# Kernel optimization log

Hardware: AMD Instinct MI355X
Metric: run time of the kernel (lower is better)

## Reference

```python
import jax, jax.numpy as jnp
import numpy as np

NNZ = 3355443          # int(4096*4096*(1-0.8))
IN_FEATURES = 4096
OUT_FEATURES = 4096
BATCH = 64
ACTIVE_THRESHOLD = 0.01


def setup_inputs() -> dict:
    key = jax.random.key(0)
    k1, k2, k3, k4 = jax.random.split(key, 4)
    x = jax.random.uniform(k1, (BATCH, IN_FEATURES), dtype=jnp.float32)
    row_indices = jax.random.randint(k2, (NNZ,), 0, OUT_FEATURES, dtype=jnp.int32)
    col_indices = jax.random.randint(k3, (NNZ,), 0, IN_FEATURES, dtype=jnp.int32)
    values = jax.random.normal(k4, (NNZ,), dtype=jnp.float32)
    bias = jnp.zeros((OUT_FEATURES,), dtype=jnp.float32)
    return {"x": x, "row_indices": row_indices, "col_indices": col_indices,
            "values": values, "bias": bias}


def reference(x, row_indices, col_indices, values, bias):
    # Event-driven gating: only columns with x > threshold contribute.
    # Equivalent to masking x, then a standard COO spmv per batch row.
    xm = jnp.where(x > ACTIVE_THRESHOLD, x, jnp.zeros((), x.dtype))   # [B, in]
    contrib = values[None, :] * xm[:, col_indices]                    # [B, nnz]
    out = jnp.zeros((x.shape[0], bias.shape[0]), dtype=x.dtype)
    out = out.at[:, row_indices].add(contrib)                         # scatter-add over rows
    return out + bias[None, :]
```

## Files before the change

### kernel.cpp

```cpp
#include <hip/hip_runtime.h>
#include <hip/hip_bf16.h>
#include <stdint.h>

#define IN_F 4096
#define OUT_F 4096
#define NBKT 512
#define SBLOCKS 410
#define REC_PER_SB 8192
#define SMAX 7168u
#define THRESH 0.01f

typedef unsigned int u32;
typedef unsigned short u16;
typedef __attribute__((ext_vector_type(8))) short short8;
typedef __attribute__((ext_vector_type(4))) float f32x4;

static constexpr size_t pad256(size_t x) { return (x + 255u) & ~(size_t)255u; }
static constexpr size_t WS_XB   = 0;
static constexpr size_t WS_CUR  = pad256(WS_XB + (size_t)512 * 64 * 8 * 2);
static constexpr size_t WS_BINS = pad256(WS_CUR + (size_t)NBKT * 4);
static constexpr size_t WS_NEEDED = WS_BINS + (size_t)NBKT * SMAX * 4;

static __device__ __forceinline__ u16 f2bf(float v) {
  __hip_bfloat16 h = __float2bfloat16(v);
  return *reinterpret_cast<u16*>(&h);
}

__global__ __launch_bounds__(512) void k_init(u32* __restrict__ gcursor) {
  gcursor[threadIdx.x] = 0u;
}

__global__ __launch_bounds__(1024) void k_scatter(const int* __restrict__ rows,
                                                  const int* __restrict__ cols,
                                                  const float* __restrict__ vals, u32 nnz,
                                                  const float* __restrict__ x,
                                                  u16* __restrict__ xB,
                                                  u32* __restrict__ gcursor,
                                                  u32* __restrict__ sortb) {
  __shared__ u32 cnt[NBKT];
  __shared__ u32 pref[NBKT + 1];
  __shared__ u32 gbase[NBKT];
  __shared__ u32 srt[REC_PER_SB];
  __shared__ u16 srtb[REC_PER_SB];
  const int tid = threadIdx.x;
  const int lane = tid & 63;
  const int wid = tid >> 6;

  if (blockIdx.x < 32) {
    const int g = blockIdx.x * 1024 + tid;
    const int b = g & 63;
    const int kg = g >> 6;
    const float* src = x + (size_t)b * IN_F + kg * 8;
    const f32x4 a0 = *reinterpret_cast<const f32x4*>(src);
    const f32x4 a1 = *reinterpret_cast<const f32x4*>(src + 4);
    short8 o;
#pragma unroll
    for (int e = 0; e < 4; ++e) {
      float v = a0[e]; v = (v > THRESH) ? v : 0.0f; o[e] = (short)f2bf(v);
    }
#pragma unroll
    for (int e = 0; e < 4; ++e) {
      float v = a1[e]; v = (v > THRESH) ? v : 0.0f; o[4 + e] = (short)f2bf(v);
    }
    *reinterpret_cast<short8*>(xB + ((size_t)kg * 64 + b) * 8) = o;
  }

  if (tid < NBKT) cnt[tid] = 0;
  __syncthreads();
  const u32 base_i = blockIdx.x * (u32)REC_PER_SB;
  u32 rec[8], bkt[8], rk[8];
#pragma unroll
  for (int j = 0; j < 8; ++j) {
    const u32 i = base_i + (u32)j * 1024u + tid;
    bkt[j] = 0xffffffffu;
    if (i < nnz) {
      const u32 r = (u32)rows[i] & 4095u;
      const u32 c = (u32)cols[i] & 4095u;
      rec[j] = (c << 20) | ((r & 7u) << 16) | (u32)f2bf(vals[i]);
      bkt[j] = r >> 3;
      rk[j] = atomicAdd(&cnt[bkt[j]], 1u);
    }
  }
  __syncthreads();
  if (wid == 0) {
    u32 a[8]; u32 s = 0;
#pragma unroll
    for (int j = 0; j < 8; ++j) { a[j] = cnt[lane * 8 + j]; s += a[j]; }
    u32 xx = s;
#pragma unroll
    for (int d = 1; d < 64; d <<= 1) {
      const u32 y = (u32)__shfl_up((int)xx, d, 64);
      if (lane >= d) xx += y;
    }
    u32 e = xx - s;
#pragma unroll
    for (int j = 0; j < 8; ++j) { pref[lane * 8 + j] = e; e += a[j]; }
    if (lane == 63) pref[NBKT] = e;
  }
  __syncthreads();
#pragma unroll
  for (int j = 0; j < 8; ++j)
    if (bkt[j] != 0xffffffffu) {
      const u32 pos = pref[bkt[j]] + rk[j];
      srt[pos] = rec[j];
      srtb[pos] = (u16)bkt[j];
    }
  if (tid < NBKT) {
    const u32 len = pref[tid + 1] - pref[tid];
    gbase[tid] = len ? atomicAdd(&gcursor[tid], len) : 0u;
  }
  __syncthreads();
  const u32 tot = pref[NBKT];
#pragma unroll
  for (int j = 0; j < 8; ++j) {
    const u32 i = (u32)j * 1024u + tid;
    if (i < tot) {
      const u32 t = srtb[i];
      const u32 off = gbase[t] + (i - pref[t]);
      if (off < SMAX) sortb[(size_t)t * SMAX + off] = srt[i];
    }
  }
}

__global__ __launch_bounds__(1024, 4) void k_accum(const u32* __restrict__ sortb,
                                                   const u32* __restrict__ ntot,
                                                   const u16* __restrict__ xB,
                                                   const float* __restrict__ bias,
                                                   float* __restrict__ out) {
  __shared__ float W[8 * 4096];
  const int tid = threadIdx.x;
  const int lane = tid & 63;
  const int w = tid >> 6;
  const u32 t = blockIdx.x;
  u32 n = ntot[t];
  if (n > SMAX) n = SMAX;
  const u32* bin = sortb + (size_t)t * SMAX;

  const f32x4 zv = {0.f, 0.f, 0.f, 0.f};
#pragma unroll
  for (int j = 0; j < 8; ++j)
    *reinterpret_cast<f32x4*>(&W[j * 4096 + tid * 4]) = zv;
  __syncthreads();

#define ADDREC(RC) do {                                                   \
    const u32 rl_ = ((RC) >> 16) & 7u;                                    \
    const u32 cl_ = ((RC) >> 20) ^ (rl_ << 3);    \
    unsafeAtomicAdd(&W[rl_ * 4096u + cl_], __uint_as_float((RC) << 16));  \
  } while (0)
  u32 i = (u32)tid;
  for (; i + 3072u < n; i += 4096u) {
    const u32 r0 = bin[i];
    const u32 r1 = bin[i + 1024u];
    const u32 r2 = bin[i + 2048u];
    const u32 r3 = bin[i + 3072u];
    ADDREC(r0); ADDREC(r1); ADDREC(r2); ADDREC(r3);
  }
  for (; i < n; i += 1024u) { const u32 r0 = bin[i]; ADDREC(r0); }
#undef ADDREC
  __syncthreads();

  f32x4 acc0 = zv, acc1 = zv, acc2 = zv, acc3 = zv;
  const int row = lane & 15;
  const bool alive = row < 8;
  const int rw = row & 7;
  const int e8 = (lane >> 4) * 8;
#pragma unroll
  for (int s = 0; s < 8; ++s) {
    const int klb = w * 256 + s * 32 + e8;
    const int sw = klb ^ (rw << 3);
    f32x4 wa = *reinterpret_cast<const f32x4*>(&W[rw * 4096 + sw]);
    f32x4 wb = *reinterpret_cast<const f32x4*>(&W[rw * 4096 + (sw + 4)]);
    if (!alive) { wa = zv; wb = zv; }
    short8 af;
#pragma unroll
    for (int e = 0; e < 4; ++e) af[e] = (short)f2bf(wa[e]);
#pragma unroll
    for (int e = 0; e < 4; ++e) af[4 + e] = (short)f2bf(wb[e]);
    const u16* bp = xB + (size_t)(klb >> 3) * 512 + (u32)row * 8;
    const short8 b0 = *reinterpret_cast<const short8*>(bp);
    const short8 b1 = *reinterpret_cast<const short8*>(bp + 128);
    const short8 b2 = *reinterpret_cast<const short8*>(bp + 256);
    const short8 b3 = *reinterpret_cast<const short8*>(bp + 384);
    acc0 = __builtin_amdgcn_mfma_f32_16x16x32_bf16(af, b0, acc0, 0, 0, 0);
    acc1 = __builtin_amdgcn_mfma_f32_16x16x32_bf16(af, b1, acc1, 0, 0, 0);
    acc2 = __builtin_amdgcn_mfma_f32_16x16x32_bf16(af, b2, acc2, 0, 0, 0);
    acc3 = __builtin_amdgcn_mfma_f32_16x16x32_bf16(af, b3, acc3, 0, 0, 0);
  }
  __syncthreads();
  {
    const int ccol = lane & 15;
    const int rb = (lane >> 4) * 4;
    if (rb < 8) {
#pragma unroll
      for (int qq = 0; qq < 4; ++qq) W[((w * 4 + 0) * 8 + rb + qq) * 16 + ccol] = acc0[qq];
#pragma unroll
      for (int qq = 0; qq < 4; ++qq) W[((w * 4 + 1) * 8 + rb + qq) * 16 + ccol] = acc1[qq];
#pragma unroll
      for (int qq = 0; qq < 4; ++qq) W[((w * 4 + 2) * 8 + rb + qq) * 16 + ccol] = acc2[qq];
#pragma unroll
      for (int qq = 0; qq < 4; ++qq) W[((w * 4 + 3) * 8 + rb + qq) * 16 + ccol] = acc3[qq];
    }
  }
  __syncthreads();
  if (tid < 512) {
    const int rl = tid & 7;
    const int b = tid >> 3;
    float sum = bias[t * 8u + rl];
#pragma unroll
    for (int w2 = 0; w2 < 16; ++w2)
      sum += W[((w2 * 4 + (b >> 4)) * 8 + rl) * 16 + (b & 15)];
    out[(size_t)b * OUT_F + t * 8u + rl] = sum;
  }
}

__global__ __launch_bounds__(256) void k_bias_init(const float* __restrict__ bias,
                                                   float* __restrict__ out) {
  const int i = blockIdx.x * 256 + threadIdx.x;
  if (i < 64 * OUT_F) out[i] = bias[i & (OUT_F - 1)];
}

__global__ __launch_bounds__(256) void k_fallback(const int* __restrict__ rows,
                                                  const int* __restrict__ cols,
                                                  const float* __restrict__ vals,
                                                  const float* __restrict__ x,
                                                  float* __restrict__ out, int nnz) {
  const int gw = (int)(((u32)blockIdx.x * blockDim.x + threadIdx.x) >> 6);
  const int lane = threadIdx.x & 63;
  const int nw = (int)(((u32)gridDim.x * blockDim.x) >> 6);
  for (int i = gw; i < nnz; i += nw) {
    const int r = rows[i];
    const int c = cols[i];
    const float v = vals[i];
    const float xv = x[lane * IN_F + c];
    if (xv > THRESH) atomicAdd(&out[(size_t)lane * OUT_F + r], v * xv);
  }
}

extern "C" void kernel_launch(void* const* d_in, const int* in_sizes, int n_in,
                              void* d_out, int out_size, void* d_ws, size_t ws_size,
                              hipStream_t stream) {
  const float* x = (const float*)d_in[0];
  const int* rows = (const int*)d_in[1];
  const int* cols = (const int*)d_in[2];
  const float* vals = (const float*)d_in[3];
  const float* bias = (const float*)d_in[4];
  float* out = (float*)d_out;
  const int nnz = in_sizes[1];

  if (ws_size >= WS_NEEDED && nnz <= SBLOCKS * REC_PER_SB) {
    u16* xB = (u16*)((char*)d_ws + WS_XB);
    u32* gcursor = (u32*)((char*)d_ws + WS_CUR);
    u32* sortb = (u32*)((char*)d_ws + WS_BINS);
    k_init<<<1, 512, 0, stream>>>(gcursor);
    k_scatter<<<SBLOCKS, 1024, 0, stream>>>(rows, cols, vals, (u32)nnz, x, xB,
                                            gcursor, sortb);
    k_accum<<<NBKT, 1024, 0, stream>>>(sortb, gcursor, xB, bias, out);
  } else {
    k_bias_init<<<(64 * OUT_F + 255) / 256, 256, 0, stream>>>(bias, out);
    k_fallback<<<4096, 256, 0, stream>>>(rows, cols, vals, x, out, nnz);
  }
}
```

Before: 59.76 us.

## Re-bin sparse entries into 64-row by 512-column tiles with split-K combine

Sparse entries are now binned by a 64-output-row by 512-input-column tile rather than by 8 full rows. Each accumulate block builds a dense 64x512 slice in LDS and runs MFMAs over all 16-row groups, which removes the half-masked MFMA rows the old 8-row layout wasted. Each block writes a partial 64x64 result to workspace, and a new combine kernel sums the 8 K-splits and adds bias. The cost is an extra kernel launch, a round trip of the partial sums through global memory, and a slightly larger per-bin capacity.

```diff
diff --git a/kernel.cpp b/kernel.cpp
--- a/kernel.cpp
+++ b/kernel.cpp
@@ -4,10 +4,10 @@
 
 #define IN_F 4096
 #define OUT_F 4096
-#define NBKT 512
+#define NBIN 512
 #define SBLOCKS 410
 #define REC_PER_SB 8192
-#define SMAX 7168u
+#define SMAX 7424u
 #define THRESH 0.01f
 
 typedef unsigned int u32;
@@ -18,16 +18,17 @@
 static constexpr size_t pad256(size_t x) { return (x + 255u) & ~(size_t)255u; }
 static constexpr size_t WS_XB   = 0;
 static constexpr size_t WS_CUR  = pad256(WS_XB + (size_t)512 * 64 * 8 * 2);
-static constexpr size_t WS_BINS = pad256(WS_CUR + (size_t)NBKT * 4);
-static constexpr size_t WS_NEEDED = WS_BINS + (size_t)NBKT * SMAX * 4;
+static constexpr size_t WS_BINS = pad256(WS_CUR + (size_t)NBIN * 4);
+static constexpr size_t WS_PART = pad256(WS_BINS + (size_t)NBIN * SMAX * 4);
+static constexpr size_t WS_NEEDED = WS_PART + (size_t)NBIN * 4096 * 4;
 
 static __device__ __forceinline__ u16 f2bf(float v) {
   __hip_bfloat16 h = __float2bfloat16(v);
   return *reinterpret_cast<u16*>(&h);
 }
 
-__global__ __launch_bounds__(512) void k_init(u32* __restrict__ gcursor) {
-  gcursor[threadIdx.x] = 0u;
+__global__ __launch_bounds__(512) void k_init(u32* __restrict__ cur) {
+  cur[threadIdx.x] = 0u;
 }
 
 __global__ __launch_bounds__(1024) void k_scatter(const int* __restrict__ rows,
@@ -37,9 +38,9 @@
                                                   u16* __restrict__ xB,
                                                   u32* __restrict__ gcursor,
                                                   u32* __restrict__ sortb) {
-  __shared__ u32 cnt[NBKT];
-  __shared__ u32 pref[NBKT + 1];
-  __shared__ u32 gbase[NBKT];
+  __shared__ u32 cnt[NBIN];
+  __shared__ u32 pref[NBIN + 1];
+  __shared__ u32 gbase[NBIN];
   __shared__ u32 srt[REC_PER_SB];
   __shared__ u16 srtb[REC_PER_SB];
   const int tid = threadIdx.x;
@@ -55,17 +56,13 @@
     const f32x4 a1 = *reinterpret_cast<const f32x4*>(src + 4);
     short8 o;
 #pragma unroll
-    for (int e = 0; e < 4; ++e) {
-      float v = a0[e]; v = (v > THRESH) ? v : 0.0f; o[e] = (short)f2bf(v);
-    }
-#pragma unroll
-    for (int e = 0; e < 4; ++e) {
-      float v = a1[e]; v = (v > THRESH) ? v : 0.0f; o[4 + e] = (short)f2bf(v);
-    }
+    for (int e = 0; e < 4; ++e) { float v = a0[e]; o[e] = (short)f2bf(v > THRESH ? v : 0.f); }
+#pragma unroll
+    for (int e = 0; e < 4; ++e) { float v = a1[e]; o[4 + e] = (short)f2bf(v > THRESH ? v : 0.f); }
     *reinterpret_cast<short8*>(xB + ((size_t)kg * 64 + b) * 8) = o;
   }
 
-  if (tid < NBKT) cnt[tid] = 0;
+  if (tid < NBIN) cnt[tid] = 0;
   __syncthreads();
   const u32 base_i = blockIdx.x * (u32)REC_PER_SB;
   u32 rec[8], bkt[8], rk[8];
@@ -76,8 +73,8 @@
     if (i < nnz) {
       const u32 r = (u32)rows[i] & 4095u;
       const u32 c = (u32)cols[i] & 4095u;
-      rec[j] = (c << 20) | ((r & 7u) << 16) | (u32)f2bf(vals[i]);
-      bkt[j] = r >> 3;
+      rec[j] = ((c & 511u) << 22) | ((r & 63u) << 16) | (u32)f2bf(vals[i]);
+      bkt[j] = ((r >> 6) << 3) | (c >> 9);
       rk[j] = atomicAdd(&cnt[bkt[j]], 1u);
     }
   }
@@ -95,7 +92,7 @@
     u32 e = xx - s;
 #pragma unroll
     for (int j = 0; j < 8; ++j) { pref[lane * 8 + j] = e; e += a[j]; }
-    if (lane == 63) pref[NBKT] = e;
+    if (lane == 63) pref[NBIN] = e;
   }
   __syncthreads();
 #pragma unroll
@@ -105,12 +102,12 @@
       srt[pos] = rec[j];
       srtb[pos] = (u16)bkt[j];
     }
-  if (tid < NBKT) {
+  if (tid < NBIN) {
     const u32 len = pref[tid + 1] - pref[tid];
     gbase[tid] = len ? atomicAdd(&gcursor[tid], len) : 0u;
   }
   __syncthreads();
-  const u32 tot = pref[NBKT];
+  const u32 tot = pref[NBIN];
 #pragma unroll
   for (int j = 0; j < 8; ++j) {
     const u32 i = (u32)j * 1024u + tid;
@@ -125,92 +122,77 @@
 __global__ __launch_bounds__(1024, 4) void k_accum(const u32* __restrict__ sortb,
                                                    const u32* __restrict__ ntot,
                                                    const u16* __restrict__ xB,
-                                                   const float* __restrict__ bias,
-                                                   float* __restrict__ out) {
-  __shared__ float W[8 * 4096];
+                                                   float* __restrict__ part) {
+  __shared__ float W[64 * 512];
+  const u32 bin = blockIdx.x;
+  const u32 rg = bin >> 3, ks = bin & 7;
+  u32 n = ntot[bin];
+  if (n > SMAX) n = SMAX;
+  const u32* bb = sortb + (size_t)bin * SMAX;
   const int tid = threadIdx.x;
   const int lane = tid & 63;
   const int w = tid >> 6;
-  const u32 t = blockIdx.x;
-  u32 n = ntot[t];
-  if (n > SMAX) n = SMAX;
-  const u32* bin = sortb + (size_t)t * SMAX;
-
   const f32x4 zv = {0.f, 0.f, 0.f, 0.f};
 #pragma unroll
   for (int j = 0; j < 8; ++j)
     *reinterpret_cast<f32x4*>(&W[j * 4096 + tid * 4]) = zv;
   __syncthreads();
-
-#define ADDREC(RC) do {                                                   \
-    const u32 rl_ = ((RC) >> 16) & 7u;                                    \
-    const u32 cl_ = ((RC) >> 20) ^ (rl_ << 3);    \
-    unsafeAtomicAdd(&W[rl_ * 4096u + cl_], __uint_as_float((RC) << 16));  \
+#define ADDREC(RC) do {                                                     \
+    const u32 rl_ = ((RC) >> 16) & 63u;                                     \
+    const u32 cl_ = (((RC) >> 22) & 511u) ^ ((rl_ & 7u) << 3);              \
+    unsafeAtomicAdd(&W[rl_ * 512u + cl_], __uint_as_float((RC) << 16));     \
   } while (0)
   u32 i = (u32)tid;
   for (; i + 3072u < n; i += 4096u) {
-    const u32 r0 = bin[i];
-    const u32 r1 = bin[i + 1024u];
-    const u32 r2 = bin[i + 2048u];
-    const u32 r3 = bin[i + 3072u];
+    const u32 r0 = bb[i], r1 = bb[i + 1024u], r2 = bb[i + 2048u], r3 = bb[i + 3072u];
     ADDREC(r0); ADDREC(r1); ADDREC(r2); ADDREC(r3);
   }
-  for (; i < n; i += 1024u) { const u32 r0 = bin[i]; ADDREC(r0); }
+  for (; i < n; i += 1024u) { const u32 r0 = bb[i]; ADDREC(r0); }
 #undef ADDREC
   __syncthreads();
-
-  f32x4 acc0 = zv, acc1 = zv, acc2 = zv, acc3 = zv;
-  const int row = lane & 15;
-  const bool alive = row < 8;
-  const int rw = row & 7;
+  const int rt = w >> 2, bg = w & 3;
+  const int fr = lane & 15;
   const int e8 = (lane >> 4) * 8;
-#pragma unroll
-  for (int s = 0; s < 8; ++s) {
-    const int klb = w * 256 + s * 32 + e8;
-    const int sw = klb ^ (rw << 3);
-    f32x4 wa = *reinterpret_cast<const f32x4*>(&W[rw * 4096 + sw]);
-    f32x4 wb = *reinterpret_cast<const f32x4*>(&W[rw * 4096 + (sw + 4)]);
-    if (!alive) { wa = zv; wb = zv; }
+  const int rl = rt * 16 + fr;
+  f32x4 acc = zv;
+  const u32 kbase = ks * 512u;
+#pragma unroll
+  for (int ck = 0; ck < 16; ++ck) {
+    const int klb = ck * 32 + e8;
+    const int sw = klb ^ ((rl & 7) << 3);
+    const f32x4 wa = *reinterpret_cast<const f32x4*>(&W[rl * 512 + sw]);
+    const f32x4 wb = *reinterpret_cast<const f32x4*>(&W[rl * 512 + sw + 4]);
     short8 af;
 #pragma unroll
     for (int e = 0; e < 4; ++e) af[e] = (short)f2bf(wa[e]);
 #pragma unroll
     for (int e = 0; e < 4; ++e) af[4 + e] = (short)f2bf(wb[e]);
-    const u16* bp = xB + (size_t)(klb >> 3) * 512 + (u32)row * 8;
-    const short8 b0 = *reinterpret_cast<const short8*>(bp);
-    const short8 b1 = *reinterpret_cast<const short8*>(bp + 128);
-    const short8 b2 = *reinterpret_cast<const short8*>(bp + 256);
-    const short8 b3 = *reinterpret_cast<const short8*>(bp + 384);
-    acc0 = __builtin_amdgcn_mfma_f32_16x16x32_bf16(af, b0, acc0, 0, 0, 0);
-    acc1 = __builtin_amdgcn_mfma_f32_16x16x32_bf16(af, b1, acc1, 0, 0, 0);
-    acc2 = __builtin_amdgcn_mfma_f32_16x16x32_bf16(af, b2, acc2, 0, 0, 0);
-    acc3 = __builtin_amdgcn_mfma_f32_16x16x32_bf16(af, b3, acc3, 0, 0, 0);
-  }
-  __syncthreads();
-  {
-    const int ccol = lane & 15;
-    const int rb = (lane >> 4) * 4;
-    if (rb < 8) {
-#pragma unroll
-      for (int qq = 0; qq < 4; ++qq) W[((w * 4 + 0) * 8 + rb + qq) * 16 + ccol] = acc0[qq];
-#pragma unroll
-      for (int qq = 0; qq < 4; ++qq) W[((w * 4 + 1) * 8 + rb + qq) * 16 + ccol] = acc1[qq];
-#pragma unroll
-      for (int qq = 0; qq < 4; ++qq) W[((w * 4 + 2) * 8 + rb + qq) * 16 + ccol] = acc2[qq];
-#pragma unroll
-      for (int qq = 0; qq < 4; ++qq) W[((w * 4 + 3) * 8 + rb + qq) * 16 + ccol] = acc3[qq];
-    }
-  }
-  __syncthreads();
-  if (tid < 512) {
-    const int rl = tid & 7;
-    const int b = tid >> 3;
-    float sum = bias[t * 8u + rl];
-#pragma unroll
-    for (int w2 = 0; w2 < 16; ++w2)
-      sum += W[((w2 * 4 + (b >> 4)) * 8 + rl) * 16 + (b & 15)];
-    out[(size_t)b * OUT_F + t * 8u + rl] = sum;
-  }
+    const u32 kabs = kbase + (u32)klb;
+    const short8 bf = *reinterpret_cast<const short8*>(
+        xB + ((size_t)(kabs >> 3) * 64 + (u32)(bg * 16 + fr)) * 8);
+    acc = __builtin_amdgcn_mfma_f32_16x16x32_bf16(af, bf, acc, 0, 0, 0);
+  }
+  __syncthreads();
+#pragma unroll
+  for (int qq = 0; qq < 4; ++qq)
+    W[(bg * 16 + fr) * 64 + rt * 16 + (lane >> 4) * 4 + qq] = acc[qq];
+  __syncthreads();
+  *reinterpret_cast<f32x4*>(&part[(size_t)bin * 4096 + tid * 4]) =
+      *reinterpret_cast<const f32x4*>(&W[tid * 4]);
+}
+
+__global__ __launch_bounds__(1024) void k_combine(const float* __restrict__ part,
+                                                  const float* __restrict__ bias,
+                                                  float* __restrict__ out) {
+  const u32 rg = blockIdx.x >> 2;
+  const u32 idx = (blockIdx.x & 3) * 1024u + threadIdx.x;
+  const u32 b = idx >> 6;
+  const u32 r = idx & 63u;
+  float sum = bias[rg * 64u + r];
+  const float* p = part + (size_t)(rg * 8u) * 4096 + idx;
+#pragma unroll
+  for (int ks = 0; ks < 8; ++ks) sum += p[(size_t)ks * 4096];
+  out[(size_t)b * OUT_F + rg * 64u + r] = sum;
 }
 
 __global__ __launch_bounds__(256) void k_bias_init(const float* __restrict__ bias,
@@ -249,12 +231,13 @@
 
   if (ws_size >= WS_NEEDED && nnz <= SBLOCKS * REC_PER_SB) {
     u16* xB = (u16*)((char*)d_ws + WS_XB);
-    u32* gcursor = (u32*)((char*)d_ws + WS_CUR);
+    u32* cur = (u32*)((char*)d_ws + WS_CUR);
     u32* sortb = (u32*)((char*)d_ws + WS_BINS);
-    k_init<<<1, 512, 0, stream>>>(gcursor);
-    k_scatter<<<SBLOCKS, 1024, 0, stream>>>(rows, cols, vals, (u32)nnz, x, xB,
-                                            gcursor, sortb);
-    k_accum<<<NBKT, 1024, 0, stream>>>(sortb, gcursor, xB, bias, out);
+    float* part = (float*)((char*)d_ws + WS_PART);
+    k_init<<<1, 512, 0, stream>>>(cur);
+    k_scatter<<<SBLOCKS, 1024, 0, stream>>>(rows, cols, vals, (u32)nnz, x, xB, cur, sortb);
+    k_accum<<<NBIN, 1024, 0, stream>>>(sortb, cur, xB, part);
+    k_combine<<<256, 1024, 0, stream>>>(part, bias, out);
   } else {
     k_bias_init<<<(64 * OUT_F + 255) / 256, 256, 0, stream>>>(bias, out);
     k_fallback<<<4096, 256, 0, stream>>>(rows, cols, vals, x, out, nnz);
```

Result: no change. 59.81 us (+0.1%).
